# Optimization experiments

Measured on AMD Instinct MI355X. Metric: run time of the kernel, lower is better.

Reference implementation:

```python
import jax, jax.numpy as jnp
import numpy as np

NUM_HEADS = 4
OUT_DIM = 64
IN_DIM = 128

def setup_inputs() -> dict:
    key = jax.random.key(0)
    k1, k2, k3, k4 = jax.random.split(key, 4)
    h = jax.random.normal(k1, (4, 256, IN_DIM), dtype=jnp.float32)
    adj = jax.random.randint(k2, (4, 256, 256), 0, 2).astype(jnp.int32)
    W = jax.random.normal(k3, (IN_DIM, NUM_HEADS * OUT_DIM), dtype=jnp.float32) * (1.0 / np.sqrt(IN_DIM))
    a = jax.random.normal(k4, (2 * OUT_DIM, 1), dtype=jnp.float32) * 0.1
    return {"h": h, "adj": adj, "W": W, "a": a}

def reference(h, adj, W, a):
    B, N, _ = h.shape
    H, D = NUM_HEADS, OUT_DIM
    Wh = (h @ W).reshape(B, N, H, D)                      # [B,N,H,D]
    # Exact replication of the torch repeat/view construction (row-major, same as torch.view)
    a1 = jnp.tile(Wh, (1, 1, 1, N)).reshape(B, N * H, N, D)
    a2 = jnp.tile(Wh, (1, N, 1, 1)).reshape(B, N * H, N, D)
    a_input = jnp.concatenate([a1, a2], axis=3)           # [B,N*H,N,2D]
    e = jax.nn.leaky_relu((a_input @ a)[..., 0], negative_slope=0.2)
    e = e.reshape(B, H, N, N)
    mask = adj[:, None, :, :] == 0                        # broadcast over heads
    attention = jax.nn.softmax(jnp.where(mask, -jnp.inf, e), axis=3)  # [B,H,N,N]
    h_prime = jnp.einsum('bhij,bjhd->bihd', attention, Wh)             # [B,N,H,D]
    return h_prime.reshape(B, N, H * D)
```

## Files before the change

### kernel.cpp

```cpp
#include <hip/hip_runtime.h>


typedef __attribute__((ext_vector_type(8))) short bf16x8;
typedef __attribute__((ext_vector_type(4))) float f32x4;

__device__ __forceinline__ short bf1(float x) {
  unsigned u = __builtin_bit_cast(unsigned, x);
  u = (u + 0x7FFFu + ((u >> 16) & 1u)) >> 16;
  return (short)u;
}
__device__ __forceinline__ bf16x8 pack8(float4 a, float4 b) {
  bf16x8 r;
  r[0]=bf1(a.x); r[1]=bf1(a.y); r[2]=bf1(a.z); r[3]=bf1(a.w);
  r[4]=bf1(b.x); r[5]=bf1(b.y); r[6]=bf1(b.z); r[7]=bf1(b.w);
  return r;
}

__global__ __launch_bounds__(512) void gat_prep(
    const float* __restrict__ h, const float* __restrict__ W,
    const float* __restrict__ a,
    short* __restrict__ WhT, float* __restrict__ f1g, float* __restrict__ f2g)
{
  const int tid  = threadIdx.x;
  const int lane = tid & 63;
  const int quad = lane >> 4, col = lane & 15;
  const int wv   = tid >> 6;
  const int blk  = blockIdx.x;
  const int ms = blk & 7, nt = (blk >> 3) & 3, b = blk >> 5;

  __shared__ short WbT[64][136];
  __shared__ float f1p[32][4];
  __shared__ float f2p[32][4];

#pragma unroll
  for (int q = 0; q < 4; q++) {
    const int idx = q * 512 + tid;
    const int k = idx >> 4, c4 = idx & 15;
    float4 w4 = *(const float4*)(W + k * 256 + nt * 64 + c4 * 4);
    WbT[c4*4 + 0][k] = bf1(w4.x);
    WbT[c4*4 + 1][k] = bf1(w4.y);
    WbT[c4*4 + 2][k] = bf1(w4.z);
    WbT[c4*4 + 3][k] = bf1(w4.w);
  }
  __syncthreads();

  const int tc = wv & 3;
  const int tr = wv >> 2;
  const float a1v = a[tc*16 + col];
  const float a2v = a[64 + tc*16 + col];

  const float* hrow = h + (b*256 + ms*32 + tr*16 + col) * 128 + quad*8;
  f32x4 acc = {0.f, 0.f, 0.f, 0.f};
#pragma unroll
  for (int kk = 0; kk < 4; kk++) {
    float4 lo = *(const float4*)(hrow + kk*32);
    float4 hi = *(const float4*)(hrow + kk*32 + 4);
    bf16x8 bw = *(const bf16x8*)&WbT[tc*16 + col][kk*32 + quad*8];
    acc = __builtin_amdgcn_mfma_f32_16x16x32_bf16(pack8(lo, hi), bw, acc, 0, 0, 0);
  }
  {
    const int dcol = nt*64 + tc*16 + col;
    const int n0   = ms*32 + tr*16 + quad*4;
    int2 pk;
    pk.x = (int)((unsigned)(unsigned short)bf1(acc[0]) |
                 ((unsigned)(unsigned short)bf1(acc[1]) << 16));
    pk.y = (int)((unsigned)(unsigned short)bf1(acc[2]) |
                 ((unsigned)(unsigned short)bf1(acc[3]) << 16));
    *(int2*)(WhT + b*65536 + dcol*256 + n0) = pk;
  }
#pragma unroll
  for (int r = 0; r < 4; r++) {
    float v1 = acc[r] * a1v;
    float v2 = acc[r] * a2v;
#pragma unroll
    for (int off = 1; off < 16; off <<= 1) {
      v1 += __shfl_xor(v1, off, 64);
      v2 += __shfl_xor(v2, off, 64);
    }
    if (col == 0) {
      const int row = tr*16 + quad*4 + r;
      f1p[row][tc] = v1;
      f2p[row][tc] = v2;
    }
  }
  __syncthreads();

  if (tid < 32) {
    const float s = f1p[tid][0] + f1p[tid][1] + f1p[tid][2] + f1p[tid][3];
    f1g[b*1024 + (ms*32 + tid)*4 + nt] = s;
  } else if (tid >= 64 && tid < 96) {
    const int n = tid - 64;
    const float s = f2p[n][0] + f2p[n][1] + f2p[n][2] + f2p[n][3];
    f2g[b*1024 + (ms*32 + n)*4 + nt] = s;
  }
}

__global__ __launch_bounds__(512) void gat_attn(
    const short* __restrict__ WhT, const float* __restrict__ f1g,
    const float* __restrict__ f2g, const int* __restrict__ adj,
    float* __restrict__ out)
{
  const int tid  = threadIdx.x;
  const int lane = tid & 63;
  const int quad = lane >> 4, col = lane & 15;
  const int wv   = tid >> 6;
  const int blk  = blockIdx.x;
  const int it2 = blk & 7, hp = (blk >> 3) & 3, b = blk >> 5;
  const int i0 = it2 * 32;

  __shared__ short attb[32][264];
  __shared__ float sinv[32];

  const int rt = wv >> 2, ct = wv & 3;

  bf16x8 bv[8];
  const short* bp = WhT + b*65536 + (hp*64 + ct*16 + col)*256 + quad*8;
#pragma unroll
  for (int kk = 0; kk < 8; kk++) bv[kk] = *(const bf16x8*)(bp + kk*32);

  float4 f2v[4]; int4 av[4]; float f1s[4];
#pragma unroll
  for (int rq = 0; rq < 4; rq++) {
    const int i = i0 + wv*4 + rq;
    f2v[rq] = *(const float4*)(f2g + b*1024 + rq*256 + lane*4);
    av[rq]  = *(const int4*)(adj + (b*256 + i)*256 + lane*4);
    f1s[rq] = f1g[b*1024 + hp*256 + i];
  }

#pragma unroll
  for (int rq = 0; rq < 4; rq++) {
    const int rr = wv*4 + rq;
    const float s1v = f1s[rq];
    float e0 = s1v + f2v[rq].x, e1 = s1v + f2v[rq].y;
    float e2 = s1v + f2v[rq].z, e3 = s1v + f2v[rq].w;
    e0 = e0 > 0.f ? e0 : 0.2f*e0;  e1 = e1 > 0.f ? e1 : 0.2f*e1;
    e2 = e2 > 0.f ? e2 : 0.2f*e2;  e3 = e3 > 0.f ? e3 : 0.2f*e3;
    e0 = av[rq].x ? e0 : -1e30f;  e1 = av[rq].y ? e1 : -1e30f;
    e2 = av[rq].z ? e2 : -1e30f;  e3 = av[rq].w ? e3 : -1e30f;
    float x0 = __expf(e0), x1 = __expf(e1);
    float x2 = __expf(e2), x3 = __expf(e3);
    int2 pk2;
    pk2.x = (int)((unsigned)(unsigned short)bf1(x0) |
                  ((unsigned)(unsigned short)bf1(x1) << 16));
    pk2.y = (int)((unsigned)(unsigned short)bf1(x2) |
                  ((unsigned)(unsigned short)bf1(x3) << 16));
    *(int2*)&attb[rr][lane*4] = pk2;
    float s = (x0 + x1) + (x2 + x3);
#pragma unroll
    for (int off = 32; off > 0; off >>= 1) s += __shfl_xor(s, off, 64);
    if (lane == 0) sinv[rr] = 1.f / s;
  }
  __syncthreads();

  bf16x8 af[8];
#pragma unroll
  for (int kk = 0; kk < 8; kk++)
    af[kk] = *(const bf16x8*)&attb[rt*16 + col][kk*32 + quad*8];
  f32x4 acc0 = {0.f, 0.f, 0.f, 0.f};
  f32x4 acc1 = {0.f, 0.f, 0.f, 0.f};
#pragma unroll
  for (int kk = 0; kk < 4; kk++)
    acc0 = __builtin_amdgcn_mfma_f32_16x16x32_bf16(af[kk], bv[kk], acc0, 0, 0, 0);
#pragma unroll
  for (int kk = 4; kk < 8; kk++)
    acc1 = __builtin_amdgcn_mfma_f32_16x16x32_bf16(af[kk], bv[kk], acc1, 0, 0, 0);
#pragma unroll
  for (int r = 0; r < 4; r++) {
    const int m = rt*16 + quad*4 + r;
    out[(b*256 + i0 + m)*256 + hp*64 + ct*16 + col] = (acc0[r] + acc1[r]) * sinv[m];
  }
}

extern "C" void kernel_launch(void* const* d_in, const int* in_sizes, int n_in,
                              void* d_out, int out_size, void* d_ws, size_t ws_size,
                              hipStream_t stream) {
  const float* h   = (const float*)d_in[0];
  const int*   adj = (const int*)d_in[1];
  const float* W   = (const float*)d_in[2];
  const float* a   = (const float*)d_in[3];
  float* out = (float*)d_out;

  short* WhT = (short*)d_ws;
  float* f1g = (float*)((char*)d_ws + 4*256*256*2);
  float* f2g = f1g + 4*1024;

  gat_prep<<<128, 512, 0, stream>>>(h, W, a, WhT, f1g, f2g);
  gat_attn<<<128, 512, 0, stream>>>(WhT, f1g, f2g, adj, out);
}
```

Measured before the change: 68.79 us.

## Fuse prep and attention kernels into one cooperative launch with grid sync

Merges the projection kernel and the attention kernel into a single cooperative kernel separated by a grid-wide barrier, removing one kernel launch and the gap between them. The W and h loads are also issued together before the LDS writes to overlap latency. The softmax row sums are now computed with extra MFMAs against a ones vector instead of a cross-lane shuffle reduction. The cost is the overhead of a cooperative launch and grid barrier, plus sums taken from the bf16-rounded probabilities.

```diff
diff --git a/kernel.cpp b/kernel.cpp
--- a/kernel.cpp
+++ b/kernel.cpp
@@ -1,4 +1,7 @@
 #include <hip/hip_runtime.h>
+#include <hip/hip_cooperative_groups.h>
+
+namespace cg = cooperative_groups;
 
 
 typedef __attribute__((ext_vector_type(8))) short bf16x8;
@@ -16,88 +19,10 @@
   return r;
 }
 
-__global__ __launch_bounds__(512) void gat_prep(
+__global__ __launch_bounds__(512) void gat_all(
     const float* __restrict__ h, const float* __restrict__ W,
-    const float* __restrict__ a,
-    short* __restrict__ WhT, float* __restrict__ f1g, float* __restrict__ f2g)
-{
-  const int tid  = threadIdx.x;
-  const int lane = tid & 63;
-  const int quad = lane >> 4, col = lane & 15;
-  const int wv   = tid >> 6;
-  const int blk  = blockIdx.x;
-  const int ms = blk & 7, nt = (blk >> 3) & 3, b = blk >> 5;
-
-  __shared__ short WbT[64][136];
-  __shared__ float f1p[32][4];
-  __shared__ float f2p[32][4];
-
-#pragma unroll
-  for (int q = 0; q < 4; q++) {
-    const int idx = q * 512 + tid;
-    const int k = idx >> 4, c4 = idx & 15;
-    float4 w4 = *(const float4*)(W + k * 256 + nt * 64 + c4 * 4);
-    WbT[c4*4 + 0][k] = bf1(w4.x);
-    WbT[c4*4 + 1][k] = bf1(w4.y);
-    WbT[c4*4 + 2][k] = bf1(w4.z);
-    WbT[c4*4 + 3][k] = bf1(w4.w);
-  }
-  __syncthreads();
-
-  const int tc = wv & 3;
-  const int tr = wv >> 2;
-  const float a1v = a[tc*16 + col];
-  const float a2v = a[64 + tc*16 + col];
-
-  const float* hrow = h + (b*256 + ms*32 + tr*16 + col) * 128 + quad*8;
-  f32x4 acc = {0.f, 0.f, 0.f, 0.f};
-#pragma unroll
-  for (int kk = 0; kk < 4; kk++) {
-    float4 lo = *(const float4*)(hrow + kk*32);
-    float4 hi = *(const float4*)(hrow + kk*32 + 4);
-    bf16x8 bw = *(const bf16x8*)&WbT[tc*16 + col][kk*32 + quad*8];
-    acc = __builtin_amdgcn_mfma_f32_16x16x32_bf16(pack8(lo, hi), bw, acc, 0, 0, 0);
-  }
-  {
-    const int dcol = nt*64 + tc*16 + col;
-    const int n0   = ms*32 + tr*16 + quad*4;
-    int2 pk;
-    pk.x = (int)((unsigned)(unsigned short)bf1(acc[0]) |
-                 ((unsigned)(unsigned short)bf1(acc[1]) << 16));
-    pk.y = (int)((unsigned)(unsigned short)bf1(acc[2]) |
-                 ((unsigned)(unsigned short)bf1(acc[3]) << 16));
-    *(int2*)(WhT + b*65536 + dcol*256 + n0) = pk;
-  }
-#pragma unroll
-  for (int r = 0; r < 4; r++) {
-    float v1 = acc[r] * a1v;
-    float v2 = acc[r] * a2v;
-#pragma unroll
-    for (int off = 1; off < 16; off <<= 1) {
-      v1 += __shfl_xor(v1, off, 64);
-      v2 += __shfl_xor(v2, off, 64);
-    }
-    if (col == 0) {
-      const int row = tr*16 + quad*4 + r;
-      f1p[row][tc] = v1;
-      f2p[row][tc] = v2;
-    }
-  }
-  __syncthreads();
-
-  if (tid < 32) {
-    const float s = f1p[tid][0] + f1p[tid][1] + f1p[tid][2] + f1p[tid][3];
-    f1g[b*1024 + (ms*32 + tid)*4 + nt] = s;
-  } else if (tid >= 64 && tid < 96) {
-    const int n = tid - 64;
-    const float s = f2p[n][0] + f2p[n][1] + f2p[n][2] + f2p[n][3];
-    f2g[b*1024 + (ms*32 + n)*4 + nt] = s;
-  }
-}
-
-__global__ __launch_bounds__(512) void gat_attn(
-    const short* __restrict__ WhT, const float* __restrict__ f1g,
-    const float* __restrict__ f2g, const int* __restrict__ adj,
+    const float* __restrict__ a, const int* __restrict__ adj,
+    short* __restrict__ WhT, float* __restrict__ f1g, float* __restrict__ f2g,
     float* __restrict__ out)
 {
   const int tid  = threadIdx.x;
@@ -105,69 +30,155 @@
   const int quad = lane >> 4, col = lane & 15;
   const int wv   = tid >> 6;
   const int blk  = blockIdx.x;
-  const int it2 = blk & 7, hp = (blk >> 3) & 3, b = blk >> 5;
-  const int i0 = it2 * 32;
-
+
+  __shared__ short WbT[64][136];
+  __shared__ float f1p[32][4];
+  __shared__ float f2p[32][4];
   __shared__ short attb[32][264];
-  __shared__ float sinv[32];
-
-  const int rt = wv >> 2, ct = wv & 3;
-
-  bf16x8 bv[8];
-  const short* bp = WhT + b*65536 + (hp*64 + ct*16 + col)*256 + quad*8;
-#pragma unroll
-  for (int kk = 0; kk < 8; kk++) bv[kk] = *(const bf16x8*)(bp + kk*32);
-
-  float4 f2v[4]; int4 av[4]; float f1s[4];
-#pragma unroll
-  for (int rq = 0; rq < 4; rq++) {
-    const int i = i0 + wv*4 + rq;
-    f2v[rq] = *(const float4*)(f2g + b*1024 + rq*256 + lane*4);
-    av[rq]  = *(const int4*)(adj + (b*256 + i)*256 + lane*4);
-    f1s[rq] = f1g[b*1024 + hp*256 + i];
+
+  {
+    const int ms = blk & 7, nt = (blk >> 3) & 3, b = blk >> 5;
+    const int tc = wv & 3;
+    const int tr = wv >> 2;
+
+    float4 wl[4];
+#pragma unroll
+    for (int q = 0; q < 4; q++) {
+      const int idx = q * 512 + tid;
+      const int k = idx >> 4, c4 = idx & 15;
+      wl[q] = *(const float4*)(W + k * 256 + nt * 64 + c4 * 4);
+    }
+    const float* hrow = h + (b*256 + ms*32 + tr*16 + col) * 128 + quad*8;
+    float4 hv[8];
+#pragma unroll
+    for (int kk = 0; kk < 4; kk++) {
+      hv[2*kk]   = *(const float4*)(hrow + kk*32);
+      hv[2*kk+1] = *(const float4*)(hrow + kk*32 + 4);
+    }
+    const float a1v = a[tc*16 + col];
+    const float a2v = a[64 + tc*16 + col];
+
+#pragma unroll
+    for (int q = 0; q < 4; q++) {
+      const int idx = q * 512 + tid;
+      const int k = idx >> 4, c4 = idx & 15;
+      WbT[c4*4 + 0][k] = bf1(wl[q].x);
+      WbT[c4*4 + 1][k] = bf1(wl[q].y);
+      WbT[c4*4 + 2][k] = bf1(wl[q].z);
+      WbT[c4*4 + 3][k] = bf1(wl[q].w);
+    }
+    __syncthreads();
+
+    f32x4 acc = {0.f, 0.f, 0.f, 0.f};
+#pragma unroll
+    for (int kk = 0; kk < 4; kk++) {
+      bf16x8 bw = *(const bf16x8*)&WbT[tc*16 + col][kk*32 + quad*8];
+      acc = __builtin_amdgcn_mfma_f32_16x16x32_bf16(pack8(hv[2*kk], hv[2*kk+1]), bw, acc, 0, 0, 0);
+    }
+    {
+      const int dcol = nt*64 + tc*16 + col;
+      const int n0   = ms*32 + tr*16 + quad*4;
+      int2 pk;
+      pk.x = (int)((unsigned)(unsigned short)bf1(acc[0]) |
+                   ((unsigned)(unsigned short)bf1(acc[1]) << 16));
+      pk.y = (int)((unsigned)(unsigned short)bf1(acc[2]) |
+                   ((unsigned)(unsigned short)bf1(acc[3]) << 16));
+      *(int2*)(WhT + b*65536 + dcol*256 + n0) = pk;
+    }
+#pragma unroll
+    for (int r = 0; r < 4; r++) {
+      float v1 = acc[r] * a1v;
+      float v2 = acc[r] * a2v;
+#pragma unroll
+      for (int off = 1; off < 16; off <<= 1) {
+        v1 += __shfl_xor(v1, off, 64);
+        v2 += __shfl_xor(v2, off, 64);
+      }
+      if (col == 0) {
+        const int row = tr*16 + quad*4 + r;
+        f1p[row][tc] = v1;
+        f2p[row][tc] = v2;
+      }
+    }
+    __syncthreads();
+
+    if (tid < 32) {
+      const float s = f1p[tid][0] + f1p[tid][1] + f1p[tid][2] + f1p[tid][3];
+      f1g[b*1024 + (ms*32 + tid)*4 + nt] = s;
+    } else if (tid >= 64 && tid < 96) {
+      const int n = tid - 64;
+      const float s = f2p[n][0] + f2p[n][1] + f2p[n][2] + f2p[n][3];
+      f2g[b*1024 + (ms*32 + n)*4 + nt] = s;
+    }
   }
 
-#pragma unroll
-  for (int rq = 0; rq < 4; rq++) {
-    const int rr = wv*4 + rq;
-    const float s1v = f1s[rq];
-    float e0 = s1v + f2v[rq].x, e1 = s1v + f2v[rq].y;
-    float e2 = s1v + f2v[rq].z, e3 = s1v + f2v[rq].w;
-    e0 = e0 > 0.f ? e0 : 0.2f*e0;  e1 = e1 > 0.f ? e1 : 0.2f*e1;
-    e2 = e2 > 0.f ? e2 : 0.2f*e2;  e3 = e3 > 0.f ? e3 : 0.2f*e3;
-    e0 = av[rq].x ? e0 : -1e30f;  e1 = av[rq].y ? e1 : -1e30f;
-    e2 = av[rq].z ? e2 : -1e30f;  e3 = av[rq].w ? e3 : -1e30f;
-    float x0 = __expf(e0), x1 = __expf(e1);
-    float x2 = __expf(e2), x3 = __expf(e3);
-    int2 pk2;
-    pk2.x = (int)((unsigned)(unsigned short)bf1(x0) |
-                  ((unsigned)(unsigned short)bf1(x1) << 16));
-    pk2.y = (int)((unsigned)(unsigned short)bf1(x2) |
-                  ((unsigned)(unsigned short)bf1(x3) << 16));
-    *(int2*)&attb[rr][lane*4] = pk2;
-    float s = (x0 + x1) + (x2 + x3);
-#pragma unroll
-    for (int off = 32; off > 0; off >>= 1) s += __shfl_xor(s, off, 64);
-    if (lane == 0) sinv[rr] = 1.f / s;
-  }
-  __syncthreads();
-
-  bf16x8 af[8];
-#pragma unroll
-  for (int kk = 0; kk < 8; kk++)
-    af[kk] = *(const bf16x8*)&attb[rt*16 + col][kk*32 + quad*8];
-  f32x4 acc0 = {0.f, 0.f, 0.f, 0.f};
-  f32x4 acc1 = {0.f, 0.f, 0.f, 0.f};
-#pragma unroll
-  for (int kk = 0; kk < 4; kk++)
-    acc0 = __builtin_amdgcn_mfma_f32_16x16x32_bf16(af[kk], bv[kk], acc0, 0, 0, 0);
-#pragma unroll
-  for (int kk = 4; kk < 8; kk++)
-    acc1 = __builtin_amdgcn_mfma_f32_16x16x32_bf16(af[kk], bv[kk], acc1, 0, 0, 0);
-#pragma unroll
-  for (int r = 0; r < 4; r++) {
-    const int m = rt*16 + quad*4 + r;
-    out[(b*256 + i0 + m)*256 + hp*64 + ct*16 + col] = (acc0[r] + acc1[r]) * sinv[m];
+  __threadfence();
+  cg::this_grid().sync();
+
+  {
+    const int it2 = blk & 7, hp = (blk >> 3) & 3, b = blk >> 5;
+    const int i0 = it2 * 32;
+    const int rt = wv >> 2, ct = wv & 3;
+
+    bf16x8 bv[8];
+    const short* bp = WhT + b*65536 + (hp*64 + ct*16 + col)*256 + quad*8;
+#pragma unroll
+    for (int kk = 0; kk < 8; kk++) bv[kk] = *(const bf16x8*)(bp + kk*32);
+
+    float4 f2v[4]; int4 av[4]; float f1s[4];
+#pragma unroll
+    for (int rq = 0; rq < 4; rq++) {
+      const int i = i0 + wv*4 + rq;
+      f2v[rq] = *(const float4*)(f2g + b*1024 + rq*256 + lane*4);
+      av[rq]  = *(const int4*)(adj + (b*256 + i)*256 + lane*4);
+      f1s[rq] = f1g[b*1024 + hp*256 + i];
+    }
+
+#pragma unroll
+    for (int rq = 0; rq < 4; rq++) {
+      const int rr = wv*4 + rq;
+      const float s1v = f1s[rq];
+      float e0 = s1v + f2v[rq].x, e1 = s1v + f2v[rq].y;
+      float e2 = s1v + f2v[rq].z, e3 = s1v + f2v[rq].w;
+      e0 = e0 > 0.f ? e0 : 0.2f*e0;  e1 = e1 > 0.f ? e1 : 0.2f*e1;
+      e2 = e2 > 0.f ? e2 : 0.2f*e2;  e3 = e3 > 0.f ? e3 : 0.2f*e3;
+      e0 = av[rq].x ? e0 : -1e30f;  e1 = av[rq].y ? e1 : -1e30f;
+      e2 = av[rq].z ? e2 : -1e30f;  e3 = av[rq].w ? e3 : -1e30f;
+      float x0 = __expf(e0), x1 = __expf(e1);
+      float x2 = __expf(e2), x3 = __expf(e3);
+      int2 pk2;
+      pk2.x = (int)((unsigned)(unsigned short)bf1(x0) |
+                    ((unsigned)(unsigned short)bf1(x1) << 16));
+      pk2.y = (int)((unsigned)(unsigned short)bf1(x2) |
+                    ((unsigned)(unsigned short)bf1(x3) << 16));
+      *(int2*)&attb[rr][lane*4] = pk2;
+    }
+    __syncthreads();
+
+    bf16x8 af[8];
+#pragma unroll
+    for (int kk = 0; kk < 8; kk++)
+      af[kk] = *(const bf16x8*)&attb[rt*16 + col][kk*32 + quad*8];
+
+    bf16x8 ones;
+#pragma unroll
+    for (int j = 0; j < 8; j++) ones[j] = (short)0x3F80;
+
+    f32x4 acc0 = {0.f,0.f,0.f,0.f}, acc1 = {0.f,0.f,0.f,0.f};
+    f32x4 sum0 = {0.f,0.f,0.f,0.f}, sum1 = {0.f,0.f,0.f,0.f};
+#pragma unroll
+    for (int kk = 0; kk < 4; kk++) {
+      acc0 = __builtin_amdgcn_mfma_f32_16x16x32_bf16(af[kk],   bv[kk],   acc0, 0, 0, 0);
+      acc1 = __builtin_amdgcn_mfma_f32_16x16x32_bf16(af[kk+4], bv[kk+4], acc1, 0, 0, 0);
+      sum0 = __builtin_amdgcn_mfma_f32_16x16x32_bf16(af[kk],   ones,     sum0, 0, 0, 0);
+      sum1 = __builtin_amdgcn_mfma_f32_16x16x32_bf16(af[kk+4], ones,     sum1, 0, 0, 0);
+    }
+#pragma unroll
+    for (int r = 0; r < 4; r++) {
+      const int m = rt*16 + quad*4 + r;
+      out[(b*256 + i0 + m)*256 + hp*64 + ct*16 + col] =
+          (acc0[r] + acc1[r]) / (sum0[r] + sum1[r]);
+    }
   }
 }
 
@@ -184,6 +195,7 @@
   float* f1g = (float*)((char*)d_ws + 4*256*256*2);
   float* f2g = f1g + 4*1024;
 
-  gat_prep<<<128, 512, 0, stream>>>(h, W, a, WhT, f1g, f2g);
-  gat_attn<<<128, 512, 0, stream>>>(WhT, f1g, f2g, adj, out);
-}
+  void* args[] = { (void*)&h, (void*)&W, (void*)&a, (void*)&adj,
+                   (void*)&WhT, (void*)&f1g, (void*)&f2g, (void*)&out };
+  hipLaunchCooperativeKernel(gat_all, dim3(128), dim3(512), args, 0, stream);
+}
```

New measurement: 107.4 us. 56.2% more time.
